# Kernel optimization log

Measured on AMD Instinct MI355X. Metric: run time of the kernel, lower is better.

The kernel has to match this reference:

```python
import jax, jax.numpy as jnp
import numpy as np

B, S, E = 2, 2048, 1024
H = 16
D = E // H  # head_dim = 64


def setup_inputs() -> dict:
    key = jax.random.key(0)
    ks = jax.random.split(key, 11)
    s = 1.0 / np.sqrt(E)
    return {
        "x": jax.random.normal(ks[0], (B, S, E), dtype=jnp.float32),
        "Wq": jax.random.uniform(ks[1], (E, E), jnp.float32, -s, s),
        "bq": jnp.zeros((E,), jnp.float32),
        "Wk": jax.random.uniform(ks[2], (E, E), jnp.float32, -s, s),
        "bk": jnp.zeros((E,), jnp.float32),
        "Wv": jax.random.uniform(ks[3], (E, E), jnp.float32, -s, s),
        "bv": jnp.zeros((E,), jnp.float32),
        "Wo": jax.random.uniform(ks[4], (E, E), jnp.float32, -s, s),
        "bo": jnp.zeros((E,), jnp.float32),
        "J_attn": jax.random.normal(ks[5], (H, D, D), jnp.float32) * 0.02,
        "lambda_attn": jnp.float32(0.5),
    }


def reference(x, Wq, bq, Wk, bk, Wv, bv, Wo, bo, J_attn, lambda_attn):
    b, s, _ = x.shape
    scale = jnp.sqrt(jnp.float32(D))

    def split_heads(y):  # [b,s,E] -> [b,H,s,D]
        return y.reshape(b, s, H, D).transpose(0, 2, 1, 3)

    Q = split_heads(x @ Wq.T + bq)
    K = split_heads(x @ Wk.T + bk)
    V = split_heads(x @ Wv.T + bv)

    attn_scores = jnp.einsum('bhid,bhjd->bhij', Q, K) / scale

    Qn = jnp.tanh(Q)
    Kn = jnp.tanh(K)
    # fold J into Qn first (small [H,D,D] contraction), then one big matmul
    QJ = jnp.einsum('bhid,hde->bhie', Qn, J_attn)
    delta = jnp.einsum('bhie,bhje->bhij', QJ, Kn)

    attn_scores = attn_scores + lambda_attn * delta
    attn_probs = jax.nn.softmax(attn_scores, axis=-1)

    out = jnp.einsum('bhij,bhjd->bhid', attn_probs, V)
    out = out.transpose(0, 2, 1, 3).reshape(b, s, E)
    return out @ Wo.T + bo
```

## Files before the change

### kernel.cpp

```cpp
#include <hip/hip_runtime.h>
#include <math.h>

#define NH 16

typedef __bf16 bf16x8 __attribute__((ext_vector_type(8)));
typedef float f32x4 __attribute__((ext_vector_type(4)));

__device__ __forceinline__ unsigned short f2bf(float f) {
  unsigned u = __float_as_uint(f);
  u += 0x7fffu + ((u >> 16) & 1u);
  return (unsigned short)(u >> 16);
}
__device__ __forceinline__ float bf2f(unsigned short h) {
  return __uint_as_float(((unsigned)h) << 16);
}
__device__ __forceinline__ float fexp2(float x) {
  return __builtin_amdgcn_exp2f(x);
}
__device__ __forceinline__ float fast_tanh16(float x) {
  return 1.f - 2.f * __builtin_amdgcn_rcpf(fexp2(16.f * x) + 1.f);
}
__device__ __forceinline__ void gl_lds16(const void* g, void* l) {
  __builtin_amdgcn_global_load_lds((const __attribute__((address_space(1))) void*)g,
                                   (__attribute__((address_space(3))) void*)l, 16, 0, 0);
}
union Frag8 { bf16x8 v; unsigned short u[8]; };
union FragU { bf16x8 v; unsigned u[4]; };
union FragQ { bf16x8 v; unsigned long long q[2]; };

__global__ __launch_bounds__(256) void prep_all(const float* __restrict__ x,
                                                const float* __restrict__ Wq,
                                                const float* __restrict__ Wk,
                                                const float* __restrict__ Wv,
                                                const float* __restrict__ Wo,
                                                const float* __restrict__ J,
                                                const float* __restrict__ lam_p,
                                                unsigned short* __restrict__ xh,
                                                unsigned short* __restrict__ wcat3,
                                                unsigned short* __restrict__ wocat,
                                                unsigned short* __restrict__ Jt)
{
  __shared__ float T[64][65];
  const int bid = blockIdx.x, tid = threadIdx.x;
  if (bid >= 8192) {
    const int h = bid - 8192;
    const float lam = lam_p[0] * 1.44269504f;
#pragma unroll
    for (int c = 0; c < 4; ++c) {
      int i = tid + c*256;
      int d = i >> 4, e4 = i & 15;
      float4 v = *(const float4*)&J[(size_t)h*4096 + d*64 + e4*4];
      T[d][e4*4+0] = v.x; T[d][e4*4+1] = v.y; T[d][e4*4+2] = v.z; T[d][e4*4+3] = v.w;
    }
    __syncthreads();
    const int e = tid >> 2, d0 = (tid & 3) * 16;
#pragma unroll
    for (int j4 = 0; j4 < 4; ++j4) {
      ushort4 o;
      o.x = f2bf(lam * T[d0+j4*4+0][e]);
      o.y = f2bf(lam * T[d0+j4*4+1][e]);
      o.z = f2bf(lam * T[d0+j4*4+2][e]);
      o.w = f2bf(lam * T[d0+j4*4+3][e]);
      *(ushort4*)&Jt[((size_t)h*64 + e)*64 + d0 + j4*4] = o;
    }
    return;
  }
  if (bid < 4096) {
    int i = bid * 256 + tid;
    float4 v = *(const float4*)&x[(size_t)i*4];
    ushort4 o;
    o.x = f2bf(v.x); o.y = f2bf(v.y); o.z = f2bf(v.z); o.w = f2bf(v.w);
    *(ushort4*)&xh[(size_t)i*4] = o;
  } else if (bid < 7168) {
    int i = (bid - 4096) * 256 + tid;
    int sel = i >> 18, loc = i & 262143;
    const float* src = (sel == 0) ? Wq : (sel == 1) ? Wk : Wv;
    float4 v = *(const float4*)&src[(size_t)loc*4];
    ushort4 o;
    o.x = f2bf(v.x); o.y = f2bf(v.y); o.z = f2bf(v.z); o.w = f2bf(v.w);
    *(ushort4*)&wcat3[(size_t)i*4] = o;
  } else {
    int i = (bid - 7168) * 256 + tid;
    int r = i >> 8, c = i & 255;
    float4 v = *(const float4*)&Wo[(size_t)r*1024 + c*4];
    ushort4 hi, lo;
    hi.x = f2bf(v.x); lo.x = f2bf(v.x - bf2f(hi.x));
    hi.y = f2bf(v.y); lo.y = f2bf(v.y - bf2f(hi.y));
    hi.z = f2bf(v.z); lo.z = f2bf(v.z - bf2f(hi.z));
    hi.w = f2bf(v.w); lo.w = f2bf(v.w - bf2f(hi.w));
    *(ushort4*)&wocat[(size_t)r*2048 + c*4]        = hi;
    *(ushort4*)&wocat[(size_t)r*2048 + 1024 + c*4] = lo;
  }
}

__global__ __launch_bounds__(256) void gemm_qkv(const unsigned short* __restrict__ A,
                                                const unsigned short* __restrict__ W,
                                                const float* __restrict__ bq,
                                                const float* __restrict__ bk,
                                                const float* __restrict__ bv,
                                                unsigned short* __restrict__ Qcat,
                                                unsigned short* __restrict__ Kcat,
                                                unsigned short* __restrict__ Vt)
{
  __shared__ unsigned short S[32768];
  const int tid = threadIdx.x, lane = tid & 63, wq = tid >> 6;
  const int l15 = lane & 15, lq = lane >> 4;
  const int n0 = blockIdx.x * 128, m0 = blockIdx.y * 128;
  const int wr = (wq & 1) * 64, wc = (wq >> 1) * 64;
  const int mode = n0 >> 10;

  f32x4 acc[4][4];
#pragma unroll
  for (int mb = 0; mb < 4; ++mb)
#pragma unroll
    for (int nb = 0; nb < 4; ++nb) { f32x4 z = {0.f,0.f,0.f,0.f}; acc[mb][nb] = z; }

  const unsigned short* mat = (wq < 2) ? A : W;
  const int rbase = (wq < 2) ? m0 : n0;
  const int srow = lane >> 3, sslot = lane & 7;

  auto STAGE = [&](int buf, int k0) {
    unsigned short* lb = S + buf*16384 + (wq >> 1) * 8192;
#pragma unroll
    for (int t = 0; t < 8; ++t) {
      int row = (wq & 1) * 64 + t*8 + srow;
      int chunk = sslot ^ (row & 7);
      gl_lds16(mat + (size_t)(rbase + row)*1024 + k0 + chunk*8,
               lb + ((wq & 1) * 64 + t*8) * 64);
    }
  };

  int cur = 0;
  STAGE(0, 0);
  __syncthreads();

  for (int k0 = 0; k0 < 1024; k0 += 64) {
    if (k0 + 64 < 1024) STAGE(cur ^ 1, k0 + 64);
    const unsigned short* Sc = S + cur*16384;
#pragma unroll
    for (int kk = 0; kk < 2; ++kk) {
      int c = kk*4 + lq;
      bf16x8 af[4], bf_[4];
#pragma unroll
      for (int mb = 0; mb < 4; ++mb) {
        int m = wr + mb*16 + l15;
        af[mb] = *(const bf16x8*)&Sc[m*64 + (c ^ (m & 7))*8];
      }
#pragma unroll
      for (int nb = 0; nb < 4; ++nb) {
        int n = wc + nb*16 + l15;
        bf_[nb] = *(const bf16x8*)&Sc[8192 + n*64 + (c ^ (n & 7))*8];
      }
#pragma unroll
      for (int mb = 0; mb < 4; ++mb)
#pragma unroll
        for (int nb = 0; nb < 4; ++nb)
          acc[mb][nb] = __builtin_amdgcn_mfma_f32_16x16x32_bf16(af[mb], bf_[nb], acc[mb][nb], 0,0,0);
    }
    __syncthreads();
    cur ^= 1;
  }

  const float* bias = (mode == 0) ? bq : (mode == 1) ? bk : bv;
  float bvv[4];
#pragma unroll
  for (int nb = 0; nb < 4; ++nb) bvv[nb] = bias[((n0 & 1023) + wc + nb*16 + l15)];

  if (mode == 2) {
#pragma unroll
    for (int mb = 0; mb < 4; ++mb) {
      int mrow = m0 + wr + mb*16 + lq*4;
      int b = mrow >> 11, s0 = mrow & 2047;
#pragma unroll
      for (int nb = 0; nb < 4; ++nb) {
        int n = (n0 & 1023) + wc + nb*16 + l15;
        int h = n >> 6, d = n & 63;
        ushort4 o;
        o.x = f2bf(acc[mb][nb][0] + bvv[nb]);
        o.y = f2bf(acc[mb][nb][1] + bvv[nb]);
        o.z = f2bf(acc[mb][nb][2] + bvv[nb]);
        o.w = f2bf(acc[mb][nb][3] + bvv[nb]);
        *(ushort4*)&Vt[((size_t)(b*NH + h)*64 + d)*2048 + s0] = o;
      }
    }
    return;
  }

#pragma unroll
  for (int mb = 0; mb < 4; ++mb) {
#pragma unroll
    for (int r = 0; r < 4; ++r) {
      int m = m0 + wr + mb*16 + lq*4 + r;
      int b = m >> 11, s = m & 2047;
#pragma unroll
      for (int nb = 0; nb < 4; ++nb) {
        float v = acc[mb][nb][r] + bvv[nb];
        int n = (n0 & 1023) + wc + nb*16 + l15;
        int h = n >> 6, d = n & 63;
        size_t row = ((size_t)(b*NH + h)*2048 + s)*128;
        if (mode == 0) {
          Qcat[row + d] = f2bf(v * 0.18033688f);
        } else {
          Kcat[row + d]      = f2bf(v);
          Kcat[row + 64 + d] = f2bf(1.f - 2.f * __builtin_amdgcn_rcpf(__expf(2.f*v) + 1.f));
        }
      }
    }
  }
}

__global__ __launch_bounds__(256) void build_qj2(unsigned short* __restrict__ Qcat,
                                                 const unsigned short* __restrict__ Jt)
{
  const int tid = threadIdx.x, lane = tid & 63, wq = tid >> 6;
  const int l15 = lane & 15, lq = lane >> 4;
  const int bh = blockIdx.y, row0 = blockIdx.x * 128;
  const int h = bh & (NH-1);

  bf16x8 jf[4][2];
#pragma unroll
  for (int nb = 0; nb < 4; ++nb)
#pragma unroll
    for (int kst = 0; kst < 2; ++kst)
      jf[nb][kst] = *(const bf16x8*)&Jt[((size_t)h*64 + nb*16 + l15)*64 + kst*32 + lq*8];

  Frag8 af[2][2];
#pragma unroll
  for (int mb = 0; mb < 2; ++mb) {
    const unsigned short* qp = Qcat + ((size_t)(bh*2048 + row0 + wq*32 + mb*16 + l15))*128 + lq*8;
#pragma unroll
    for (int kst = 0; kst < 2; ++kst) {
      Frag8 raw;
      raw.v = *(const bf16x8*)(qp + kst*32);
#pragma unroll
      for (int j = 0; j < 8; ++j) {
        float t = fast_tanh16(bf2f(raw.u[j]));
        af[mb][kst].u[j] = (unsigned short)(__float_as_uint(t) >> 16);
      }
    }
  }

  f32x4 acc[2][4];
#pragma unroll
  for (int mb = 0; mb < 2; ++mb)
#pragma unroll
    for (int nb = 0; nb < 4; ++nb) { f32x4 z = {0.f,0.f,0.f,0.f}; acc[mb][nb] = z; }
#pragma unroll
  for (int kst = 0; kst < 2; ++kst)
#pragma unroll
    for (int mb = 0; mb < 2; ++mb)
#pragma unroll
      for (int nb = 0; nb < 4; ++nb)
        acc[mb][nb] = __builtin_amdgcn_mfma_f32_16x16x32_bf16(af[mb][kst].v, jf[nb][kst], acc[mb][nb], 0,0,0);

#pragma unroll
  for (int mb = 0; mb < 2; ++mb)
#pragma unroll
    for (int r = 0; r < 4; ++r) {
      size_t rowb = ((size_t)(bh*2048 + row0 + wq*32 + mb*16 + lq*4 + r))*128 + 64;
#pragma unroll
      for (int nb = 0; nb < 4; ++nb)
        Qcat[rowb + nb*16 + l15] = f2bf(acc[mb][nb][r]);
    }
}

__global__ __launch_bounds__(256, 4) void flash8(
    const unsigned short* __restrict__ Qcat, const unsigned short* __restrict__ Kcat,
    const unsigned short* __restrict__ Vt, unsigned short* __restrict__ attcat)
{
  __shared__ __align__(16) char smem[24576];
  unsigned short* Ks = (unsigned short*)smem;
  unsigned short* Vs = (unsigned short*)(smem + 16384);
  const int tid = threadIdx.x, lane = tid & 63, wq = tid >> 6;
  const int l15 = lane & 15, lq = lane >> 4;
  const int bid = blockIdx.x;
  const int bh = (((bid >> 3) & 3) << 3) | (bid & 7);
  const int inner = bid >> 5;
  const int row0 = inner * 128;

  Frag8 qf[2][4];
#pragma unroll
  for (int nb = 0; nb < 2; ++nb) {
    const unsigned short* qp = Qcat + ((size_t)(bh*2048 + row0 + wq*32 + nb*16 + l15))*128 + lq*8;
#pragma unroll
    for (int kst = 0; kst < 4; ++kst)
      qf[nb][kst].v = *(const bf16x8*)(qp + kst*32);
  }

  FragU ones;
  ones.u[0] = 0x3F803F80u; ones.u[1] = 0x3F803F80u;
  ones.u[2] = 0x3F803F80u; ones.u[3] = 0x3F803F80u;

  f32x4 o[4][2];
  f32x4 lacc[2];
  { f32x4 z = {0.f,0.f,0.f,0.f}; lacc[0] = z; lacc[1] = z; }
#pragma unroll
  for (int db = 0; db < 4; ++db)
#pragma unroll
    for (int nb = 0; nb < 2; ++nb) { f32x4 z = {0.f,0.f,0.f,0.f}; o[db][nb] = z; }

  const unsigned short* kgb = Kcat + ((size_t)bh*2048)*128;
  const unsigned short* vg  = Vt + (size_t)bh*64*2048;

  for (int jt = 0; jt < 32; ++jt) {
    __syncthreads();
#pragma unroll
    for (int t = 0; t < 4; ++t) {
      int g = (wq*4 + t)*4 + (lane >> 4);
      int slot = lane & 15;
      int chunk = (slot & 8) | ((slot ^ g) & 7);
      gl_lds16(kgb + (size_t)(jt*64 + g)*128 + chunk*8, Ks + (wq*4 + t)*512);
    }
#pragma unroll
    for (int t = 0; t < 2; ++t) {
      int rv = (wq*2 + t)*8 + (lane >> 3);
      int chunk = (lane & 7) ^ (rv & 7);
      gl_lds16(vg + (size_t)rv*2048 + jt*64 + chunk*8, Vs + (wq*2 + t)*512);
    }
    __syncthreads();

#pragma unroll
    for (int t = 0; t < 2; ++t) {
      unsigned P2[2][2][2];
#pragma unroll
      for (int kk = 0; kk < 2; ++kk) {
        const int kb = 2*t + kk;
        bf16x8 af[4];
#pragma unroll
        for (int kst = 0; kst < 4; ++kst) {
          int key = kb*16 + l15;
          int c = kst*4 + lq;
          int slot = (c & 8) | ((c ^ key) & 7);
          af[kst] = *(const bf16x8*)&Ks[key*128 + slot*8];
        }
        f32x4 s[2];
        { f32x4 z = {0.f,0.f,0.f,0.f}; s[0] = z; s[1] = z; }
        __builtin_amdgcn_s_setprio(1);
#pragma unroll
        for (int kst = 0; kst < 4; ++kst) {
          s[0] = __builtin_amdgcn_mfma_f32_16x16x32_bf16(af[kst], qf[0][kst].v, s[0], 0,0,0);
          s[1] = __builtin_amdgcn_mfma_f32_16x16x32_bf16(af[kst], qf[1][kst].v, s[1], 0,0,0);
        }
        __builtin_amdgcn_s_setprio(0);
#pragma unroll
        for (int nb = 0; nb < 2; ++nb) {
          float e0 = fexp2(s[nb][0]), e1 = fexp2(s[nb][1]);
          float e2 = fexp2(s[nb][2]), e3 = fexp2(s[nb][3]);
          P2[nb][kk][0] = __builtin_amdgcn_perm(__float_as_uint(e1), __float_as_uint(e0), 0x07060302u);
          P2[nb][kk][1] = __builtin_amdgcn_perm(__float_as_uint(e3), __float_as_uint(e2), 0x07060302u);
        }
      }

      FragU bfr[2];
#pragma unroll
      for (int nb = 0; nb < 2; ++nb) {
        bfr[nb].u[0] = P2[nb][0][0];
        bfr[nb].u[1] = P2[nb][0][1];
        bfr[nb].u[2] = P2[nb][1][0];
        bfr[nb].u[3] = P2[nb][1][1];
      }
      __builtin_amdgcn_s_setprio(1);
      lacc[0] = __builtin_amdgcn_mfma_f32_16x16x32_bf16(ones.v, bfr[0].v, lacc[0], 0,0,0);
      lacc[1] = __builtin_amdgcn_mfma_f32_16x16x32_bf16(ones.v, bfr[1].v, lacc[1], 0,0,0);

      const int c0 = 4*t + (lq >> 1);
      const int woff = 4*(lq & 1);
#pragma unroll
      for (int db = 0; db < 4; ++db) {
        int d = db*16 + l15;
        FragQ va;
        va.q[0] = *(const unsigned long long*)&Vs[d*64 + ((c0     ^ (d & 7))*8) + woff];
        va.q[1] = *(const unsigned long long*)&Vs[d*64 + (((c0+2) ^ (d & 7))*8) + woff];
        o[db][0] = __builtin_amdgcn_mfma_f32_16x16x32_bf16(va.v, bfr[0].v, o[db][0], 0,0,0);
        o[db][1] = __builtin_amdgcn_mfma_f32_16x16x32_bf16(va.v, bfr[1].v, o[db][1], 0,0,0);
      }
      __builtin_amdgcn_s_setprio(0);
    }
  }

  const int b = bh >> 4, h = bh & (NH-1);
  const float inv0 = 1.f / lacc[0][0];
  const float inv1 = 1.f / lacc[1][0];
  float* Ts = (float*)smem;
#pragma unroll
  for (int half = 0; half < 2; ++half) {
    __syncthreads();
    if ((wq >> 1) == half) {
#pragma unroll
      for (int nb = 0; nb < 2; ++nb) {
        const float inv = nb ? inv1 : inv0;
        const int rl = (wq & 1)*32 + nb*16 + l15;
#pragma unroll
        for (int db = 0; db < 4; ++db)
#pragma unroll
          for (int r = 0; r < 4; ++r)
            Ts[rl*65 + db*16 + lq*4 + r] = o[db][nb][r] * inv;
      }
    }
    __syncthreads();
    const int sl = tid >> 2, d0 = (tid & 3) * 16;
    const int srow = row0 + half*64 + sl;
    const size_t rb = ((size_t)(b*2048 + srow))*2048 + h*64;
#pragma unroll
    for (int j4 = 0; j4 < 4; ++j4) {
      float v0 = Ts[sl*65 + d0 + j4*4 + 0];
      float v1 = Ts[sl*65 + d0 + j4*4 + 1];
      float v2 = Ts[sl*65 + d0 + j4*4 + 2];
      float v3 = Ts[sl*65 + d0 + j4*4 + 3];
      ushort4 hi, lo;
      hi.x = f2bf(v0); lo.x = f2bf(v0 - bf2f(hi.x));
      hi.y = f2bf(v1); lo.y = f2bf(v1 - bf2f(hi.y));
      hi.z = f2bf(v2); lo.z = f2bf(v2 - bf2f(hi.z));
      hi.w = f2bf(v3); lo.w = f2bf(v3 - bf2f(hi.w));
      *(ushort4*)&attcat[rb + d0 + j4*4]        = hi;
      *(ushort4*)&attcat[rb + 1024 + d0 + j4*4] = lo;
    }
  }
}

__global__ __launch_bounds__(512) void gemm3b(const unsigned short* __restrict__ A,
                                              const unsigned short* __restrict__ W,
                                              const float* __restrict__ bias,
                                              float* __restrict__ out)
{
  __shared__ unsigned short S[65536];
  const int tid = threadIdx.x, lane = tid & 63, wid = tid >> 6;
  const int l15 = lane & 15, lq = lane >> 4;
  const int n0 = blockIdx.x * 128, m0 = blockIdx.y * 128;
  const int wrow = wid >> 2, wcol = wid & 3;

  f32x4 acc[4][2];
#pragma unroll
  for (int mb = 0; mb < 4; ++mb)
#pragma unroll
    for (int nb = 0; nb < 2; ++nb) { f32x4 z = {0.f,0.f,0.f,0.f}; acc[mb][nb] = z; }

  const int region = wid >> 1;
  const unsigned short* mat = (region < 2) ? A : W;
  const int rbase = (region < 2) ? m0 : n0;
  const int koff  = (region & 1) * 1024;
  const int rhalf = (wid & 1) * 64;
  const int srow = lane >> 3, sslot = lane & 7;

  auto STAGE = [&](int buf, int k0) {
    unsigned short* lb = S + buf*32768 + region*8192 + rhalf*64;
#pragma unroll
    for (int t = 0; t < 8; ++t) {
      int row = rhalf + t*8 + srow;
      int chunk = sslot ^ (row & 7);
      gl_lds16(mat + (size_t)(rbase + row)*2048 + koff + k0 + chunk*8,
               lb + t*512);
    }
  };

  int cur = 0;
  STAGE(0, 0);
  __syncthreads();

  for (int k0 = 0; k0 < 1024; k0 += 64) {
    if (k0 + 64 < 1024) STAGE(cur ^ 1, k0 + 64);
    const unsigned short* Sc = S + cur*32768;
#pragma unroll
    for (int kk = 0; kk < 2; ++kk) {
      int c = kk*4 + lq;
      bf16x8 ah[4], al[4], bh_[2], bl_[2];
#pragma unroll
      for (int mb = 0; mb < 4; ++mb) {
        int m = wrow*64 + mb*16 + l15;
        int so = (c ^ (m & 7))*8;
        ah[mb] = *(const bf16x8*)&Sc[m*64 + so];
        al[mb] = *(const bf16x8*)&Sc[8192 + m*64 + so];
      }
#pragma unroll
      for (int nb = 0; nb < 2; ++nb) {
        int n = wcol*32 + nb*16 + l15;
        int so = (c ^ (n & 7))*8;
        bh_[nb] = *(const bf16x8*)&Sc[16384 + n*64 + so];
        bl_[nb] = *(const bf16x8*)&Sc[24576 + n*64 + so];
      }
#pragma unroll
      for (int mb = 0; mb < 4; ++mb)
#pragma unroll
        for (int nb = 0; nb < 2; ++nb) {
          acc[mb][nb] = __builtin_amdgcn_mfma_f32_16x16x32_bf16(ah[mb], bh_[nb], acc[mb][nb], 0,0,0);
          acc[mb][nb] = __builtin_amdgcn_mfma_f32_16x16x32_bf16(al[mb], bh_[nb], acc[mb][nb], 0,0,0);
          acc[mb][nb] = __builtin_amdgcn_mfma_f32_16x16x32_bf16(ah[mb], bl_[nb], acc[mb][nb], 0,0,0);
        }
    }
    __syncthreads();
    cur ^= 1;
  }

  float bvv[2];
#pragma unroll
  for (int nb = 0; nb < 2; ++nb) bvv[nb] = bias[n0 + wcol*32 + nb*16 + l15];
#pragma unroll
  for (int mb = 0; mb < 4; ++mb)
#pragma unroll
    for (int r = 0; r < 4; ++r) {
      int m = m0 + wrow*64 + mb*16 + lq*4 + r;
#pragma unroll
      for (int nb = 0; nb < 2; ++nb) {
        int n = n0 + wcol*32 + nb*16 + l15;
        out[(size_t)m*1024 + n] = acc[mb][nb][r] + bvv[nb];
      }
    }
}

extern "C" void kernel_launch(void* const* d_in, const int* in_sizes, int n_in,
                              void* d_out, int out_size, void* d_ws, size_t ws_size,
                              hipStream_t stream)
{
  const float* x   = (const float*)d_in[0];
  const float* Wq  = (const float*)d_in[1];
  const float* bq  = (const float*)d_in[2];
  const float* Wk  = (const float*)d_in[3];
  const float* bk  = (const float*)d_in[4];
  const float* Wv  = (const float*)d_in[5];
  const float* bv  = (const float*)d_in[6];
  const float* Wo  = (const float*)d_in[7];
  const float* bo  = (const float*)d_in[8];
  const float* J   = (const float*)d_in[9];
  const float* lam = (const float*)d_in[10];

  char* p = (char*)d_ws;
  unsigned short* xh     = (unsigned short*)p;  p += (size_t)4096*1024*2;
  unsigned short* wcat3  = (unsigned short*)p;  p += (size_t)3072*1024*2;
  unsigned short* Jt     = (unsigned short*)p;  p += (size_t)16*64*64*2;
  p += (size_t)2*1024*1024;
  unsigned short* Qcat   = (unsigned short*)p;  p += (size_t)65536*128*2;
  unsigned short* Kcat   = (unsigned short*)p;  p += (size_t)65536*128*2;
  unsigned short* Vt     = (unsigned short*)p;  p += (size_t)32*64*2048*2;
  unsigned short* wocat  = (unsigned short*)p;  p += (size_t)1024*2048*2;
  unsigned short* attcat = (unsigned short*)p;  p += (size_t)4096*2048*2;
  float* out = (float*)d_out;

  dim3 blk(256);

  prep_all<<<dim3(8208), blk, 0, stream>>>(x, Wq, Wk, Wv, Wo, J, lam, xh, wcat3, wocat, Jt);
  gemm_qkv<<<dim3(24, 32), blk, 0, stream>>>(xh, wcat3, bq, bk, bv, Qcat, Kcat, Vt);
  build_qj2<<<dim3(16, 32), blk, 0, stream>>>(Qcat, Jt);
  flash8<<<dim3(512), blk, 0, stream>>>(Qcat, Kcat, Vt, attcat);
  gemm3b<<<dim3(8, 32), dim3(512), 0, stream>>>(attcat, wocat, bo, out);
}
```

Measured before the change: 225.0 us.

## Fuse QJ projection into QKV GEMM epilogue and double-buffer flash K/V tiles

Removes the separate build_qj2 launch: the Q-mode epilogue of gemm_qkv now stages the scaled bf16 Q tile in LDS, applies tanh, and multiplies by J with MFMA before writing the QJ half of Qcat. This avoids a kernel launch and a global re-read of Q. Separately, flash8 now double-buffers K/V tiles in LDS, prefetching the next tile while computing the current one and dropping one barrier per iteration. The LDS footprint doubles to 48KB, which may lower occupancy under the 4-blocks launch bound.

```diff
diff --git a/kernel.cpp b/kernel.cpp
--- a/kernel.cpp
+++ b/kernel.cpp
@@ -98,6 +98,7 @@
                                                 const float* __restrict__ bq,
                                                 const float* __restrict__ bk,
                                                 const float* __restrict__ bv,
+                                                const unsigned short* __restrict__ Jt,
                                                 unsigned short* __restrict__ Qcat,
                                                 unsigned short* __restrict__ Kcat,
                                                 unsigned short* __restrict__ Vt)
@@ -186,6 +187,28 @@
     return;
   }
 
+  if (mode == 1) {
+#pragma unroll
+    for (int mb = 0; mb < 4; ++mb) {
+#pragma unroll
+      for (int r = 0; r < 4; ++r) {
+        int m = m0 + wr + mb*16 + lq*4 + r;
+        int b = m >> 11, s = m & 2047;
+#pragma unroll
+        for (int nb = 0; nb < 4; ++nb) {
+          float v = acc[mb][nb][r] + bvv[nb];
+          int n = (n0 & 1023) + wc + nb*16 + l15;
+          int h = n >> 6, d = n & 63;
+          size_t row = ((size_t)(b*NH + h)*2048 + s)*128;
+          Kcat[row + d]      = f2bf(v);
+          Kcat[row + 64 + d] = f2bf(1.f - 2.f * __builtin_amdgcn_rcpf(__expf(2.f*v) + 1.f));
+        }
+      }
+    }
+    return;
+  }
+
+  unsigned short* T = S + wq * 4608;
 #pragma unroll
   for (int mb = 0; mb < 4; ++mb) {
 #pragma unroll
@@ -197,80 +220,59 @@
         float v = acc[mb][nb][r] + bvv[nb];
         int n = (n0 & 1023) + wc + nb*16 + l15;
         int h = n >> 6, d = n & 63;
-        size_t row = ((size_t)(b*NH + h)*2048 + s)*128;
-        if (mode == 0) {
-          Qcat[row + d] = f2bf(v * 0.18033688f);
-        } else {
-          Kcat[row + d]      = f2bf(v);
-          Kcat[row + 64 + d] = f2bf(1.f - 2.f * __builtin_amdgcn_rcpf(__expf(2.f*v) + 1.f));
-        }
-      }
-    }
-  }
-}
-
-__global__ __launch_bounds__(256) void build_qj2(unsigned short* __restrict__ Qcat,
-                                                 const unsigned short* __restrict__ Jt)
-{
-  const int tid = threadIdx.x, lane = tid & 63, wq = tid >> 6;
-  const int l15 = lane & 15, lq = lane >> 4;
-  const int bh = blockIdx.y, row0 = blockIdx.x * 128;
-  const int h = bh & (NH-1);
-
-  bf16x8 jf[4][2];
-#pragma unroll
-  for (int nb = 0; nb < 4; ++nb)
+        unsigned short qb = f2bf(v * 0.18033688f);
+        Qcat[((size_t)(b*NH + h)*2048 + s)*128 + d] = qb;
+        T[(mb*16 + lq*4 + r)*72 + d] = qb;
+      }
+    }
+  }
+  const int h = ((n0 & 1023) + wc) >> 6;
+  bf16x8 jf2[4][2];
+#pragma unroll
+  for (int nb2 = 0; nb2 < 4; ++nb2)
 #pragma unroll
     for (int kst = 0; kst < 2; ++kst)
-      jf[nb][kst] = *(const bf16x8*)&Jt[((size_t)h*64 + nb*16 + l15)*64 + kst*32 + lq*8];
-
-  Frag8 af[2][2];
-#pragma unroll
-  for (int mb = 0; mb < 2; ++mb) {
-    const unsigned short* qp = Qcat + ((size_t)(bh*2048 + row0 + wq*32 + mb*16 + l15))*128 + lq*8;
+      jf2[nb2][kst] = *(const bf16x8*)&Jt[((size_t)h*64 + nb2*16 + l15)*64 + kst*32 + lq*8];
+#pragma unroll
+  for (int mb = 0; mb < 4; ++mb) {
+    Frag8 af2[2];
 #pragma unroll
     for (int kst = 0; kst < 2; ++kst) {
       Frag8 raw;
-      raw.v = *(const bf16x8*)(qp + kst*32);
+      raw.v = *(const bf16x8*)&T[(mb*16 + l15)*72 + kst*32 + lq*8];
 #pragma unroll
       for (int j = 0; j < 8; ++j) {
         float t = fast_tanh16(bf2f(raw.u[j]));
-        af[mb][kst].u[j] = (unsigned short)(__float_as_uint(t) >> 16);
-      }
-    }
-  }
-
-  f32x4 acc[2][4];
-#pragma unroll
-  for (int mb = 0; mb < 2; ++mb)
-#pragma unroll
-    for (int nb = 0; nb < 4; ++nb) { f32x4 z = {0.f,0.f,0.f,0.f}; acc[mb][nb] = z; }
-#pragma unroll
-  for (int kst = 0; kst < 2; ++kst)
-#pragma unroll
-    for (int mb = 0; mb < 2; ++mb)
-#pragma unroll
-      for (int nb = 0; nb < 4; ++nb)
-        acc[mb][nb] = __builtin_amdgcn_mfma_f32_16x16x32_bf16(af[mb][kst].v, jf[nb][kst], acc[mb][nb], 0,0,0);
-
-#pragma unroll
-  for (int mb = 0; mb < 2; ++mb)
+        af2[kst].u[j] = (unsigned short)(__float_as_uint(t) >> 16);
+      }
+    }
+    f32x4 a2[4];
+#pragma unroll
+    for (int nb2 = 0; nb2 < 4; ++nb2) { f32x4 z = {0.f,0.f,0.f,0.f}; a2[nb2] = z; }
+#pragma unroll
+    for (int kst = 0; kst < 2; ++kst)
+#pragma unroll
+      for (int nb2 = 0; nb2 < 4; ++nb2)
+        a2[nb2] = __builtin_amdgcn_mfma_f32_16x16x32_bf16(af2[kst].v, jf2[nb2][kst], a2[nb2], 0,0,0);
+    int mrow = m0 + wr + mb*16 + lq*4;
+    int b = mrow >> 11, s0 = mrow & 2047;
 #pragma unroll
     for (int r = 0; r < 4; ++r) {
-      size_t rowb = ((size_t)(bh*2048 + row0 + wq*32 + mb*16 + lq*4 + r))*128 + 64;
-#pragma unroll
-      for (int nb = 0; nb < 4; ++nb)
-        Qcat[rowb + nb*16 + l15] = f2bf(acc[mb][nb][r]);
-    }
+      size_t rowb = ((size_t)(b*NH + h)*2048 + s0 + r)*128 + 64;
+#pragma unroll
+      for (int nb2 = 0; nb2 < 4; ++nb2)
+        Qcat[rowb + nb2*16 + l15] = f2bf(a2[nb2][r]);
+    }
+  }
 }
 
 __global__ __launch_bounds__(256, 4) void flash8(
     const unsigned short* __restrict__ Qcat, const unsigned short* __restrict__ Kcat,
     const unsigned short* __restrict__ Vt, unsigned short* __restrict__ attcat)
 {
-  __shared__ __align__(16) char smem[24576];
+  __shared__ __align__(16) char smem[49152];
   unsigned short* Ks = (unsigned short*)smem;
-  unsigned short* Vs = (unsigned short*)(smem + 16384);
+  unsigned short* Vs = (unsigned short*)(smem + 32768);
   const int tid = threadIdx.x, lane = tid & 63, wq = tid >> 6;
   const int l15 = lane & 15, lq = lane >> 4;
   const int bid = blockIdx.x;
@@ -302,22 +304,30 @@
   const unsigned short* kgb = Kcat + ((size_t)bh*2048)*128;
   const unsigned short* vg  = Vt + (size_t)bh*64*2048;
 
-  for (int jt = 0; jt < 32; ++jt) {
-    __syncthreads();
+  auto STAGE = [&](int buf, int jt) {
 #pragma unroll
     for (int t = 0; t < 4; ++t) {
       int g = (wq*4 + t)*4 + (lane >> 4);
       int slot = lane & 15;
       int chunk = (slot & 8) | ((slot ^ g) & 7);
-      gl_lds16(kgb + (size_t)(jt*64 + g)*128 + chunk*8, Ks + (wq*4 + t)*512);
+      gl_lds16(kgb + (size_t)(jt*64 + g)*128 + chunk*8, Ks + buf*8192 + (wq*4 + t)*512);
     }
 #pragma unroll
     for (int t = 0; t < 2; ++t) {
       int rv = (wq*2 + t)*8 + (lane >> 3);
       int chunk = (lane & 7) ^ (rv & 7);
-      gl_lds16(vg + (size_t)rv*2048 + jt*64 + chunk*8, Vs + (wq*2 + t)*512);
-    }
-    __syncthreads();
+      gl_lds16(vg + (size_t)rv*2048 + jt*64 + chunk*8, Vs + buf*4096 + (wq*2 + t)*512);
+    }
+  };
+
+  int cur = 0;
+  STAGE(0, 0);
+  __syncthreads();
+
+  for (int jt = 0; jt < 32; ++jt) {
+    if (jt + 1 < 32) STAGE(cur ^ 1, jt + 1);
+    const unsigned short* ksb = Ks + cur*8192;
+    const unsigned short* vsb = Vs + cur*4096;
 
 #pragma unroll
     for (int t = 0; t < 2; ++t) {
@@ -331,7 +341,7 @@
           int key = kb*16 + l15;
           int c = kst*4 + lq;
           int slot = (c & 8) | ((c ^ key) & 7);
-          af[kst] = *(const bf16x8*)&Ks[key*128 + slot*8];
+          af[kst] = *(const bf16x8*)&ksb[key*128 + slot*8];
         }
         f32x4 s[2];
         { f32x4 z = {0.f,0.f,0.f,0.f}; s[0] = z; s[1] = z; }
@@ -369,13 +379,16 @@
       for (int db = 0; db < 4; ++db) {
         int d = db*16 + l15;
         FragQ va;
-        va.q[0] = *(const unsigned long long*)&Vs[d*64 + ((c0     ^ (d & 7))*8) + woff];
-        va.q[1] = *(const unsigned long long*)&Vs[d*64 + (((c0+2) ^ (d & 7))*8) + woff];
+        va.q[0] = *(const unsigned long long*)&vsb[d*64 + ((c0     ^ (d & 7))*8) + woff];
+        va.q[1] = *(const unsigned long long*)&vsb[d*64 + (((c0+2) ^ (d & 7))*8) + woff];
         o[db][0] = __builtin_amdgcn_mfma_f32_16x16x32_bf16(va.v, bfr[0].v, o[db][0], 0,0,0);
         o[db][1] = __builtin_amdgcn_mfma_f32_16x16x32_bf16(va.v, bfr[1].v, o[db][1], 0,0,0);
       }
       __builtin_amdgcn_s_setprio(0);
     }
+
+    __syncthreads();
+    cur ^= 1;
   }
 
   const int b = bh >> 4, h = bh & (NH-1);
@@ -538,8 +551,7 @@
   dim3 blk(256);
 
   prep_all<<<dim3(8208), blk, 0, stream>>>(x, Wq, Wk, Wv, Wo, J, lam, xh, wcat3, wocat, Jt);
-  gemm_qkv<<<dim3(24, 32), blk, 0, stream>>>(xh, wcat3, bq, bk, bv, Qcat, Kcat, Vt);
-  build_qj2<<<dim3(16, 32), blk, 0, stream>>>(Qcat, Jt);
+  gemm_qkv<<<dim3(24, 32), blk, 0, stream>>>(xh, wcat3, bq, bk, bv, Jt, Qcat, Kcat, Vt);
   flash8<<<dim3(512), blk, 0, stream>>>(Qcat, Kcat, Vt, attcat);
   gemm3b<<<dim3(8, 32), dim3(512), 0, stream>>>(attcat, wocat, bo, out);
 }
```

After: 221.5 us. No clear change (-1.6%).
